# Kernel tuning notes

Hardware: AMD Instinct MI355X
Metric: run time of the kernel (lower is better)

Reference implementation:

```python
import jax, jax.numpy as jnp
import numpy as np

EPS = 1e-5

def dwconv(x, w):
    # x: (B,C,T), w: (C,1,3) depthwise, stride 1, pad 1
    return jax.lax.conv_general_dilated(
        x, w, window_strides=(1,), padding=[(1, 1)],
        dimension_numbers=('NCH', 'OIH', 'NCH'),
        feature_group_count=x.shape[1])

def chan_ln(x, w, b):
    # LayerNorm over channel dim (axis=1) of (B,C,T)
    mu = jnp.mean(x, axis=1, keepdims=True)
    r = x - mu
    sigma = jnp.mean(r * r, axis=1, keepdims=True)
    return (r / jnp.sqrt(sigma + EPS)) * w + b

def conv1x1(x, w, b):
    # x: (B,C,T), w: (O,C), b: (O,)
    return jnp.einsum('oc,bct->bot', w, x) + b[None, :, None]

def setup_inputs() -> dict:
    B, C, T, H = 4, 1024, 1024, 16
    key0 = jax.random.key(0)
    ks = jax.random.split(key0, 16)
    s = 0.02
    inp = {
        'query': jax.random.normal(ks[0], (B, C, T), jnp.float32),
        'key': jax.random.normal(ks[1], (B, C, T), jnp.float32),
        'value': jax.random.normal(ks[2], (B, C, T), jnp.float32),
        'query_mask': jnp.ones((B, 1, T), jnp.bool_),
        'kv_mask': jnp.ones((B, 1, T), jnp.bool_),
        # depthwise conv weights (C,1,3), no bias
        'qconv_w': jax.random.normal(ks[3], (C, 1, 3), jnp.float32) * s,
        'kconv_w': jax.random.normal(ks[4], (C, 1, 3), jnp.float32) * s,
        'vconv_w': jax.random.normal(ks[5], (C, 1, 3), jnp.float32) * s,
        # channel LayerNorm affine params (1,C,1)
        'qn_w': jnp.ones((1, C, 1), jnp.float32), 'qn_b': jnp.zeros((1, C, 1), jnp.float32),
        'kn_w': jnp.ones((1, C, 1), jnp.float32), 'kn_b': jnp.zeros((1, C, 1), jnp.float32),
        'vn_w': jnp.ones((1, C, 1), jnp.float32), 'vn_b': jnp.zeros((1, C, 1), jnp.float32),
        # 1x1 conv (= per-timestep linear) weights (C,C) + bias (C,)
        'wq': jax.random.normal(ks[6], (C, C), jnp.float32) * s, 'bq': jnp.zeros((C,), jnp.float32),
        'wk': jax.random.normal(ks[7], (C, C), jnp.float32) * s, 'bk': jnp.zeros((C,), jnp.float32),
        'wv': jax.random.normal(ks[8], (C, C), jnp.float32) * s, 'bv': jnp.zeros((C,), jnp.float32),
        'wp': jax.random.normal(ks[9], (C, C), jnp.float32) * s, 'bp': jnp.zeros((C,), jnp.float32),
    }
    return inp

def reference(query, key, value, query_mask, kv_mask,
              qconv_w, kconv_w, vconv_w,
              qn_w, qn_b, kn_w, kn_b, vn_w, vn_b,
              wq, bq, wk, bk, wv, bv, wp, bp):
    B, C, T = query.shape
    H = 16
    ch = C // H
    scale = 1.0 / jnp.sqrt(jnp.asarray(ch, query.dtype))
    qm = query_mask.astype(query.dtype)   # (B,1,T), stride 1 -> qx_mask == query_mask
    kvm = kv_mask.astype(query.dtype)

    q = chan_ln(dwconv(query, qconv_w) * qm, qn_w, qn_b)
    k = chan_ln(dwconv(key, kconv_w) * kvm, kn_w, kn_b)
    v = chan_ln(dwconv(value, vconv_w) * kvm, vn_w, vn_b)

    q = conv1x1(q, wq, bq)
    k = conv1x1(k, wk, bk)
    v = conv1x1(v, wv, bv)

    # (B,C,T) -> (B,H,T,ch)
    q = q.reshape(B, H, ch, T).transpose(0, 1, 3, 2)
    k = k.reshape(B, H, ch, T).transpose(0, 1, 3, 2)
    v = v.reshape(B, H, ch, T).transpose(0, 1, 3, 2)

    att = jax.nn.softmax(jnp.einsum('bhsc,bhtc->bhst', q, k) * scale, axis=-1)
    # post-softmax mask applied to V (not to scores) — faithful to the original
    vm = v * kvm[:, :, :, None]           # (B,1,T)->(B,1,T,1) broadcast over heads/ch
    out = jnp.einsum('bhst,bhtc->bhsc', att, vm)

    out = out.transpose(0, 1, 3, 2).reshape(B, C, T)
    out = conv1x1(out, wp, bp) * qm
    return out, query_mask
```

## Files before the change

kernel.cpp:

```cpp
#include <hip/hip_runtime.h>
#include <math.h>

#define B_ 4
#define C_ 1024
#define T_ 1024
#define H_ 16
#define CH_ 64
#define BCT (B_ * C_ * T_)

typedef __attribute__((ext_vector_type(8))) short s16x8;
typedef __attribute__((ext_vector_type(4))) float f32x4;
typedef unsigned short u16;

#define MFMA16(a, b, c) __builtin_amdgcn_mfma_f32_16x16x32_bf16((a), (b), (c), 0, 0, 0)

extern "C" __device__ float __ocml_native_exp2_f32(float);

__device__ __forceinline__ u16 f2bf(float f) {
    union { float f; unsigned u; } v; v.f = f;
    unsigned r = (v.u + 0x7fffu + ((v.u >> 16) & 1u)) >> 16;
    return (u16)r;
}
__device__ __forceinline__ float bf2f(u16 h) {
    union { unsigned u; float f; } v; v.u = (unsigned)h << 16; return v.f;
}

typedef __attribute__((address_space(3))) unsigned int lds_u32;
typedef __attribute__((address_space(1))) const unsigned int glb_u32;
__device__ __forceinline__ void glds16(const void* g, const void* l_wave_uniform) {
    __builtin_amdgcn_global_load_lds(
        (glb_u32*)(unsigned long long)g,
        (lds_u32*)(unsigned long long)l_wave_uniform, 16, 0, 0);
}

#define WAIT_BARRIER(N)                                   \
    asm volatile("s_waitcnt vmcnt(" #N ")" ::: "memory"); \
    __builtin_amdgcn_s_barrier();                         \
    __builtin_amdgcn_sched_barrier(0)

__global__ __launch_bounds__(512) void prep_kernel(
    const float* __restrict__ xq, const float* __restrict__ xk, const float* __restrict__ xv,
    const float* __restrict__ wq3, const float* __restrict__ wk3, const float* __restrict__ wv3,
    const int* __restrict__ qm, const int* __restrict__ kvm,
    const float* __restrict__ qnw, const float* __restrict__ qnb,
    const float* __restrict__ knw, const float* __restrict__ knb,
    const float* __restrict__ vnw, const float* __restrict__ vnb,
    u16* __restrict__ oq, u16* __restrict__ ok, u16* __restrict__ ov,
    const float* __restrict__ w0, const float* __restrict__ w1,
    const float* __restrict__ w2, const float* __restrict__ w3,
    u16* __restrict__ o0, u16* __restrict__ o1, u16* __restrict__ o2, u16* __restrict__ o3,
    float* __restrict__ tail_out, int ntail)
{
    __shared__ __align__(16) u16 tile[32 * 1032];
    __shared__ float red1[16][33], red2[16][33];
    __shared__ float musL[32], rssL[32];

    const int bid = blockIdx.x;
    if (bid >= 384) {
        if (bid >= 2432) {
            int i = (bid - 2432) * 512 + threadIdx.x;
            if (i < ntail) tail_out[i] = (qm[i] != 0) ? 1.f : 0.f;
            return;
        }
        const int b2 = bid - 384;
        const int mat = b2 >> 9;
        const float* __restrict__ w = (mat == 0) ? w0 : (mat == 1) ? w1 : (mat == 2) ? w2 : w3;
        u16* __restrict__ o = (mat == 0) ? o0 : (mat == 1) ? o1 : (mat == 2) ? o2 : o3;
        const int i = ((b2 & 511) * 512 + threadIdx.x) * 4;
        float4 v = *(const float4*)&w[i];
        uint2 p;
        p.x = (unsigned)f2bf(v.x) | ((unsigned)f2bf(v.y) << 16);
        p.y = (unsigned)f2bf(v.z) | ((unsigned)f2bf(v.w) << 16);
        *(uint2*)&o[i] = p;
        return;
    }

    const int z = bid >> 5;
    const int tensor = z >> 2, b = z & 3;
    const float* __restrict__ x   = (tensor == 0) ? xq  : (tensor == 1) ? xk  : xv;
    const float* __restrict__ w3c = (tensor == 0) ? wq3 : (tensor == 1) ? wk3 : wv3;
    const int* __restrict__ msk   = (tensor == 0) ? qm  : kvm;
    const float* __restrict__ wln = (tensor == 0) ? qnw : (tensor == 1) ? knw : vnw;
    const float* __restrict__ bln = (tensor == 0) ? qnb : (tensor == 1) ? knb : vnb;
    u16* __restrict__ xt = (tensor == 0) ? oq : (tensor == 1) ? ok : ov;

    const int t0 = (bid & 31) * 32;

    const int tl = threadIdx.x & 31, cs = threadIdx.x >> 5;
    const int t = t0 + tl;
    const float mk = (msk[b * T_ + t] != 0) ? 1.f : 0.f;

    float s1 = 0.f, s2 = 0.f;
    #pragma unroll 4
    for (int i = 0; i < 32; ++i) {
        const int c = 2 * (cs + 16 * i);
        const float* xr0 = x + ((size_t)(b * C_ + c)) * T_ + t;
        const float* xr1 = xr0 + T_;
        float xc0 = xr0[0];
        float xm0 = (t > 0)      ? xr0[-1] : 0.f;
        float xp0 = (t < T_ - 1) ? xr0[1]  : 0.f;
        float v0 = (w3c[3 * c + 0] * xm0 + w3c[3 * c + 1] * xc0 + w3c[3 * c + 2] * xp0) * mk;
        float xc1 = xr1[0];
        float xm1 = (t > 0)      ? xr1[-1] : 0.f;
        float xp1 = (t < T_ - 1) ? xr1[1]  : 0.f;
        float v1 = (w3c[3 * c + 3] * xm1 + w3c[3 * c + 4] * xc1 + w3c[3 * c + 5] * xp1) * mk;
        s1 += v0 + v1;
        s2 += v0 * v0 + v1 * v1;
        *(unsigned*)&tile[tl * 1032 + c] =
            (unsigned)f2bf(v0) | ((unsigned)f2bf(v1) << 16);
    }
    red1[cs][tl] = s1;
    red2[cs][tl] = s2;
    __syncthreads();
    if (threadIdx.x < 32) {
        float a = 0.f, q2 = 0.f;
        #pragma unroll
        for (int i = 0; i < 16; ++i) { a += red1[i][threadIdx.x]; q2 += red2[i][threadIdx.x]; }
        float m_  = a  * (1.f / C_);
        float var = q2 * (1.f / C_) - m_ * m_;
        musL[threadIdx.x] = m_;
        rssL[threadIdx.x] = rsqrtf(var + 1e-5f);
    }
    __syncthreads();

    #pragma unroll
    for (int it = 0; it < 8; ++it) {
        const int idx = it * 512 + threadIdx.x;
        const int tt = idx >> 7, c0 = (idx & 127) * 8;
        const s16x8 pv = *(const s16x8*)&tile[tt * 1032 + c0];
        const float m_ = musL[tt], rv = rssL[tt];
        const float4 w0v = *(const float4*)&wln[c0];
        const float4 w1v = *(const float4*)&wln[c0 + 4];
        const float4 b0v = *(const float4*)&bln[c0];
        const float4 b1v = *(const float4*)&bln[c0 + 4];
        uint4 o;
        float f0, f1;
        f0 = (bf2f((u16)pv[0]) - m_) * rv * w0v.x + b0v.x;
        f1 = (bf2f((u16)pv[1]) - m_) * rv * w0v.y + b0v.y;
        o.x = (unsigned)f2bf(f0) | ((unsigned)f2bf(f1) << 16);
        f0 = (bf2f((u16)pv[2]) - m_) * rv * w0v.z + b0v.z;
        f1 = (bf2f((u16)pv[3]) - m_) * rv * w0v.w + b0v.w;
        o.y = (unsigned)f2bf(f0) | ((unsigned)f2bf(f1) << 16);
        f0 = (bf2f((u16)pv[4]) - m_) * rv * w1v.x + b1v.x;
        f1 = (bf2f((u16)pv[5]) - m_) * rv * w1v.y + b1v.y;
        o.z = (unsigned)f2bf(f0) | ((unsigned)f2bf(f1) << 16);
        f0 = (bf2f((u16)pv[6]) - m_) * rv * w1v.z + b1v.z;
        f1 = (bf2f((u16)pv[7]) - m_) * rv * w1v.w + b1v.w;
        o.w = (unsigned)f2bf(f0) | ((unsigned)f2bf(f1) << 16);
        *(uint4*)&xt[((size_t)(b * T_ + t0 + tt)) * C_ + c0] = o;
    }
}

__device__ __forceinline__ void stage_slab(
    const u16* __restrict__ gA, const u16* __restrict__ gB,
    u16* lA, u16* lB, int k0, int wave, int lane)
{
    const int rw = lane >> 2, ch = lane & 3;
    const int sw = ((ch ^ ((rw >> 1) & 3)) * 8) + k0;
    const int r0 = 16 * wave + rw, r1 = r0 + 64;
    glds16(gA + (size_t)r0 * C_ + sw, lA + (16 * wave) * 32);
    glds16(gA + (size_t)r1 * C_ + sw, lA + (64 + 16 * wave) * 32);
    glds16(gB + (size_t)r0 * C_ + sw, lB + (16 * wave) * 32);
    glds16(gB + (size_t)r1 * C_ + sw, lB + (64 + 16 * wave) * 32);
}

template<int OUT_BF16>
__device__ __forceinline__ void gemm_core(
    const u16* __restrict__ A, const u16* __restrict__ B, void* __restrict__ D,
    const float* __restrict__ bias, const int* __restrict__ mask,
    float scale, int bias_on_n, int m0, int n0)
{
    __shared__ __align__(16) u16 As[3][128 * 32];
    __shared__ __align__(16) u16 Bs[3][128 * 32];
    const int tid = threadIdx.x, lane = tid & 63, wave = tid >> 6;
    const int r = lane & 15, g = lane >> 4;
    const int wm = (wave >> 1) * 64, wn = (wave & 1) * 64;
    const u16* Ab = A + (size_t)m0 * C_;
    const u16* Bb = B + (size_t)n0 * C_;

    f32x4 acc[4][4];
    #pragma unroll
    for (int i = 0; i < 4; ++i)
        #pragma unroll
        for (int j = 0; j < 4; ++j) acc[i][j] = f32x4{0.f, 0.f, 0.f, 0.f};

    stage_slab(Ab, Bb, As[0], Bs[0], 0, wave, lane);
    stage_slab(Ab, Bb, As[1], Bs[1], 32, wave, lane);
    WAIT_BARRIER(4);

    const int swz = (g ^ ((r >> 1) & 3)) * 8;
    const int NK = C_ / 32;
    int cur = 0;
    for (int kk = 0; kk < NK; ++kk) {
        int pre = cur + 2; if (pre >= 3) pre -= 3;
        if (kk + 2 < NK)
            stage_slab(Ab, Bb, As[pre], Bs[pre], (kk + 2) * 32, wave, lane);
        s16x8 af[4], bf[4];
        #pragma unroll
        for (int mi = 0; mi < 4; ++mi)
            af[mi] = *(const s16x8*)&As[cur][(wm + 16 * mi + r) * 32 + swz];
        #pragma unroll
        for (int ni = 0; ni < 4; ++ni)
            bf[ni] = *(const s16x8*)&Bs[cur][(wn + 16 * ni + r) * 32 + swz];
        #pragma unroll
        for (int mi = 0; mi < 4; ++mi)
            #pragma unroll
            for (int ni = 0; ni < 4; ++ni)
                acc[mi][ni] = MFMA16(af[mi], bf[ni], acc[mi][ni]);
        if (kk + 1 < NK) {
            if (kk + 2 < NK) { WAIT_BARRIER(4); }
            else             { WAIT_BARRIER(0); }
        }
        cur = (cur == 2) ? 0 : cur + 1;
    }

    #pragma unroll
    for (int mi = 0; mi < 4; ++mi) {
        #pragma unroll
        for (int ni = 0; ni < 4; ++ni) {
            const int n = n0 + wn + 16 * ni + r;
            float mk = 1.f;
            if (mask) mk = (mask[n] != 0) ? 1.f : 0.f;
            #pragma unroll
            for (int i = 0; i < 4; ++i) {
                const int m = m0 + wm + 16 * mi + 4 * g + i;
                float v = acc[mi][ni][i] + (bias_on_n ? bias[n] : bias[m]);
                v *= scale * mk;
                size_t o = (size_t)m * 1024 + n;
                if (OUT_BF16) ((u16*)D)[o] = f2bf(v);
                else          ((float*)D)[o] = v;
            }
        }
    }
}

__global__ __launch_bounds__(256) void gemm_qkv_kernel(
    const u16* __restrict__ Xq, const u16* __restrict__ Xk, const u16* __restrict__ Xv,
    const u16* __restrict__ Wq, const u16* __restrict__ Wk, const u16* __restrict__ Wv,
    const float* __restrict__ bq, const float* __restrict__ bk, const float* __restrict__ bv,
    u16* __restrict__ Qt, u16* __restrict__ Kt, u16* __restrict__ Vb, const int* __restrict__ kvm)
{
    const int p = blockIdx.x;
    const int lb = (p & 7) * 96 + (p >> 3);
    const int z = lb >> 6, yy = (lb >> 3) & 7, xx = lb & 7;
    const int tensor = z >> 2, b = z & 3;
    const size_t off = (size_t)b * (1024 * 1024);
    const float qscale = 0.125f * 1.44269504088896340736f;
    const u16* A = (tensor == 0) ? Xq + off : (tensor == 1) ? Xk + off : Wv;
    const u16* B = (tensor == 0) ? Wq       : (tensor == 1) ? Wk       : Xv + off;
    u16*       D = (tensor == 0) ? Qt + off : (tensor == 1) ? Kt + off : Vb + off;
    const float* bias = (tensor == 0) ? bq : (tensor == 1) ? bk : bv;
    const int* mask = (tensor == 2) ? kvm + (size_t)b * T_ : nullptr;
    gemm_core<1>(A, B, D, bias, mask, (tensor == 0) ? qscale : 1.f, tensor != 2,
                 yy * 128, xx * 128);
}

__global__ __launch_bounds__(256) void gemm_out_kernel(
    const u16* __restrict__ Wp, const u16* __restrict__ att,
    const float* __restrict__ bp, float* __restrict__ out, const int* __restrict__ qm)
{
    const int p = blockIdx.x;
    const int lb = (p & 7) * 32 + (p >> 3);
    const int b = lb >> 6, yy = (lb >> 3) & 7, xx = lb & 7;
    const size_t off = (size_t)b * (1024 * 1024);
    gemm_core<0>(Wp, att + off, out + off, bp, qm + (size_t)b * T_, 1.f, 0,
                 yy * 128, xx * 128);
}

__global__ __launch_bounds__(256) void attn_mfma_kernel(
    const u16* __restrict__ Qt, const u16* __restrict__ Kt, const u16* __restrict__ Vb,
    u16* __restrict__ att)
{
    const int p = blockIdx.x;
    const int lb = (p & 7) * 64 + (p >> 3);
    const int bh = lb >> 3, sblk = lb & 7;
    const int b = bh >> 4, h = bh & 15;
    const int lane = threadIdx.x & 63, wave = threadIdx.x >> 6;
    const int r = lane & 15, g = lane >> 4;
    const int hofs = h * 64;
    const int s0 = sblk * 128 + wave * 16;

    __shared__ __align__(16) u16 Ks[3][64 * 64];
    __shared__ __align__(16) u16 Vs[3][64 * 64];
    __shared__ __align__(16) u16 P_lds[4][2][16 * 72];

    const u16* qb0 = Qt + ((size_t)(b * T_ + s0 + r)) * C_ + hofs + g * 8;
    const s16x8 qf00 = *(const s16x8*)(qb0);
    const s16x8 qf01 = *(const s16x8*)(qb0 + 32);
    const s16x8 qf10 = *(const s16x8*)(qb0 + (size_t)64 * C_);
    const s16x8 qf11 = *(const s16x8*)(qb0 + (size_t)64 * C_ + 32);

    const int srow = lane >> 3, sch = lane & 7;
    const u16* kg = Kt + ((size_t)(b * T_)) * C_ + hofs;
    const u16* vg = Vb + ((size_t)(b * C_ + hofs)) * T_;

    auto stage = [&](int buf, int t0) {
        #pragma unroll
        for (int i = 0; i < 2; ++i) {
            const int rr = 16 * wave + 8 * i + srow;
            const int sw = (sch ^ (rr & 7)) * 8;
            glds16(kg + (size_t)(t0 + rr) * C_ + sw, &Ks[buf][(16 * wave + 8 * i) * 64]);
            glds16(vg + (size_t)rr * T_ + t0 + sw,   &Vs[buf][(16 * wave + 8 * i) * 64]);
        }
    };

    f32x4 acc0[4], acc1[4];
    #pragma unroll
    for (int ci = 0; ci < 4; ++ci) {
        acc0[ci] = f32x4{0.f, 0.f, 0.f, 0.f};
        acc1[ci] = f32x4{0.f, 0.f, 0.f, 0.f};
    }
    float l0 = 0.f, l1 = 0.f;
    u16* pw0 = &P_lds[wave][0][0];
    u16* pw1 = &P_lds[wave][1][0];

    stage(0, 0);
    stage(1, 64);
    WAIT_BARRIER(4);

    const int NT = T_ / 64;
    int cur = 0;
    for (int it = 0; it < NT; ++it) {
        int pre = cur + 2; if (pre >= 3) pre -= 3;
        if (it + 2 < NT) stage(pre, (it + 2) * 64);

        const u16* ks = Ks[cur];
        f32x4 st0[4], st1[4];
        #pragma unroll
        for (int tt = 0; tt < 4; ++tt) {
            const int row = (16 * tt + r) * 64;
            const s16x8 ka = *(const s16x8*)&ks[row + ((g ^ (r & 7)) * 8)];
            const s16x8 kb = *(const s16x8*)&ks[row + (((4 + g) ^ (r & 7)) * 8)];
            f32x4 sa = f32x4{0.f, 0.f, 0.f, 0.f};
            sa = MFMA16(ka, qf00, sa); sa = MFMA16(kb, qf01, sa); st0[tt] = sa;
            f32x4 sb = f32x4{0.f, 0.f, 0.f, 0.f};
            sb = MFMA16(ka, qf10, sb); sb = MFMA16(kb, qf11, sb); st1[tt] = sb;
        }

        #pragma unroll
        for (int tt = 0; tt < 4; ++tt) {
            float a0 = __ocml_native_exp2_f32(st0[tt][0]);
            float a1 = __ocml_native_exp2_f32(st0[tt][1]);
            float a2 = __ocml_native_exp2_f32(st0[tt][2]);
            float a3 = __ocml_native_exp2_f32(st0[tt][3]);
            l0 += (a0 + a1) + (a2 + a3);
            uint2 pk;
            pk.x = (unsigned)f2bf(a0) | ((unsigned)f2bf(a1) << 16);
            pk.y = (unsigned)f2bf(a2) | ((unsigned)f2bf(a3) << 16);
            *(uint2*)&pw0[r * 72 + 16 * tt + 4 * g] = pk;
            float b0 = __ocml_native_exp2_f32(st1[tt][0]);
            float b1 = __ocml_native_exp2_f32(st1[tt][1]);
            float b2 = __ocml_native_exp2_f32(st1[tt][2]);
            float b3 = __ocml_native_exp2_f32(st1[tt][3]);
            l1 += (b0 + b1) + (b2 + b3);
            pk.x = (unsigned)f2bf(b0) | ((unsigned)f2bf(b1) << 16);
            pk.y = (unsigned)f2bf(b2) | ((unsigned)f2bf(b3) << 16);
            *(uint2*)&pw1[r * 72 + 16 * tt + 4 * g] = pk;
        }

        const u16* vs = Vs[cur];
        #pragma unroll
        for (int kk = 0; kk < 2; ++kk) {
            const s16x8 pa0 = *(const s16x8*)&pw0[r * 72 + 32 * kk + 8 * g];
            const s16x8 pa1 = *(const s16x8*)&pw1[r * 72 + 32 * kk + 8 * g];
            #pragma unroll
            for (int ci = 0; ci < 4; ++ci) {
                const s16x8 vf = *(const s16x8*)
                    &vs[(16 * ci + r) * 64 + (((4 * kk + g) ^ (r & 7)) * 8)];
                acc0[ci] = MFMA16(pa0, vf, acc0[ci]);
                acc1[ci] = MFMA16(pa1, vf, acc1[ci]);
            }
        }

        if (it + 1 < NT) {
            if (it + 2 < NT) { WAIT_BARRIER(4); }
            else             { WAIT_BARRIER(0); }
        }
        cur = (cur == 2) ? 0 : cur + 1;
    }

    l0 += __shfl_xor(l0, 16); l0 += __shfl_xor(l0, 32);
    l1 += __shfl_xor(l1, 16); l1 += __shfl_xor(l1, 32);
    const float inv0 = 1.f / l0, inv1 = 1.f / l1;
    const float i00 = __shfl(inv0, 4 * g + 0), i01 = __shfl(inv0, 4 * g + 1);
    const float i02 = __shfl(inv0, 4 * g + 2), i03 = __shfl(inv0, 4 * g + 3);
    const float i10 = __shfl(inv1, 4 * g + 0), i11 = __shfl(inv1, 4 * g + 1);
    const float i12 = __shfl(inv1, 4 * g + 2), i13 = __shfl(inv1, 4 * g + 3);

    u16* ob = att + ((size_t)(b * T_ + s0 + 4 * g)) * C_ + hofs + r;
    #pragma unroll
    for (int ci = 0; ci < 4; ++ci) {
        ob[(size_t)0 * C_ + ci * 16] = f2bf(acc0[ci][0] * i00);
        ob[(size_t)1 * C_ + ci * 16] = f2bf(acc0[ci][1] * i01);
        ob[(size_t)2 * C_ + ci * 16] = f2bf(acc0[ci][2] * i02);
        ob[(size_t)3 * C_ + ci * 16] = f2bf(acc0[ci][3] * i03);
    }
    u16* ob1 = ob + (size_t)64 * C_;
    #pragma unroll
    for (int ci = 0; ci < 4; ++ci) {
        ob1[(size_t)0 * C_ + ci * 16] = f2bf(acc1[ci][0] * i10);
        ob1[(size_t)1 * C_ + ci * 16] = f2bf(acc1[ci][1] * i11);
        ob1[(size_t)2 * C_ + ci * 16] = f2bf(acc1[ci][2] * i12);
        ob1[(size_t)3 * C_ + ci * 16] = f2bf(acc1[ci][3] * i13);
    }
}

extern "C" void kernel_launch(void* const* d_in, const int* in_sizes, int n_in,
                              void* d_out, int out_size, void* d_ws, size_t ws_size,
                              hipStream_t stream)
{
    const float* query = (const float*)d_in[0];
    const float* key_  = (const float*)d_in[1];
    const float* value = (const float*)d_in[2];
    const int* qm  = (const int*)d_in[3];
    const int* kvm = (const int*)d_in[4];
    const float* qconv = (const float*)d_in[5];
    const float* kconv = (const float*)d_in[6];
    const float* vconv = (const float*)d_in[7];
    const float* qnw = (const float*)d_in[8];
    const float* qnb = (const float*)d_in[9];
    const float* knw = (const float*)d_in[10];
    const float* knb = (const float*)d_in[11];
    const float* vnw = (const float*)d_in[12];
    const float* vnb = (const float*)d_in[13];
    const float* wq = (const float*)d_in[14];
    const float* bq = (const float*)d_in[15];
    const float* wk = (const float*)d_in[16];
    const float* bk = (const float*)d_in[17];
    const float* wv = (const float*)d_in[18];
    const float* bv = (const float*)d_in[19];
    const float* wp = (const float*)d_in[20];
    const float* bp = (const float*)d_in[21];

    const size_t MB = 1024 * 1024;
    char* W = (char*)d_ws;
    u16* Xq  = (u16*)(W + 0 * MB);
    u16* Xk  = (u16*)(W + 8 * MB);
    u16* Xv  = (u16*)(W + 16 * MB);
    u16* Qt  = (u16*)(W + 24 * MB);
    u16* Kt  = (u16*)(W + 32 * MB);
    u16* Vb_ = (u16*)(W + 40 * MB);
    u16* att_ = (u16*)(W + 48 * MB);
    u16* wqb = (u16*)(W + 56 * MB);
    u16* wkb = (u16*)(W + 58 * MB);
    u16* wvb = (u16*)(W + 60 * MB);
    u16* wpb = (u16*)(W + 62 * MB);

    int ntail = out_size - BCT;
    if (ntail < 0) ntail = 0;

    prep_kernel<<<dim3(2440), 512, 0, stream>>>(
        query, key_, value, qconv, kconv, vconv, qm, kvm,
        qnw, qnb, knw, knb, vnw, vnb, Xq, Xk, Xv,
        wq, wk, wv, wp, wqb, wkb, wvb, wpb,
        (float*)d_out + BCT, ntail);

    gemm_qkv_kernel<<<dim3(768), 256, 0, stream>>>(
        Xq, Xk, Xv, wqb, wkb, wvb, bq, bk, bv, Qt, Kt, Vb_, kvm);

    attn_mfma_kernel<<<dim3(512), 256, 0, stream>>>(Qt, Kt, Vb_, att_);

    gemm_out_kernel<<<dim3(256), 256, 0, stream>>>(wpb, att_, bp, (float*)d_out, qm);
}
```

Measured before the change: 122.3 us.

## Replace QKV projection GEMM with 256x256-tile 512-thread kernel over flattened batch

```diff
diff --git a/kernel.cpp b/kernel.cpp
--- a/kernel.cpp
+++ b/kernel.cpp
@@ -35,6 +35,10 @@
 
 #define WAIT_BARRIER(N)                                   \
     asm volatile("s_waitcnt vmcnt(" #N ")" ::: "memory"); \
+    __builtin_amdgcn_s_barrier();                         \
+    __builtin_amdgcn_sched_barrier(0)
+
+#define BARRIER_ONLY()                                    \
     __builtin_amdgcn_s_barrier();                         \
     __builtin_amdgcn_sched_barrier(0)
 
@@ -151,6 +155,141 @@
     }
 }
 
+__global__ __launch_bounds__(512, 2) void gemm_qkv256_kernel(
+    const u16* __restrict__ Xq, const u16* __restrict__ Xk, const u16* __restrict__ Xv,
+    const u16* __restrict__ Wq, const u16* __restrict__ Wk, const u16* __restrict__ Wv,
+    const float* __restrict__ bq, const float* __restrict__ bk, const float* __restrict__ bv,
+    u16* __restrict__ Qt, u16* __restrict__ Kt, u16* __restrict__ Vb,
+    const int* __restrict__ kvm)
+{
+    const int p = blockIdx.x;
+    const int lb = (p & 7) * 24 + (p >> 3);
+    const int tensor = lb >> 6, tidx = lb & 63;
+
+    const float qscale = 0.125f * 1.44269504088896340736f;
+    const u16 *A, *Bm; u16* Dp; const float* bias; const int* mask;
+    float scale; int bias_on_n; long ldd; int m0, n0;
+    if (tensor == 0) {
+        A = Xq; Bm = Wq; Dp = Qt; bias = bq; mask = nullptr;
+        scale = qscale; bias_on_n = 1; ldd = 1024;
+        m0 = (tidx >> 2) * 256; n0 = (tidx & 3) * 256;
+    } else if (tensor == 1) {
+        A = Xk; Bm = Wk; Dp = Kt; bias = bk; mask = nullptr;
+        scale = 1.f; bias_on_n = 1; ldd = 1024;
+        m0 = (tidx >> 2) * 256; n0 = (tidx & 3) * 256;
+    } else {
+        A = Wv; Bm = Xv; Dp = Vb; bias = bv; mask = kvm;
+        scale = 1.f; bias_on_n = 0; ldd = 4096;
+        m0 = (tidx & 3) * 256; n0 = (tidx >> 2) * 256;
+    }
+
+    __shared__ __align__(16) u16 LA[2][2][128 * 64];
+    __shared__ __align__(16) u16 LB[2][2][128 * 64];
+
+    const int tid = threadIdx.x, lane = tid & 63, wave = tid >> 6;
+    const int r = lane & 15, g = lane >> 4;
+    const int wm = (wave >> 2) * 128;
+    const int wn = (wave & 3) * 64;
+    const int ha = wave >> 2;
+    const int hb = (wave & 3) >> 1;
+    const int rbB = wn & 64;
+
+    const u16* gA = A + (size_t)m0 * 1024;
+    const u16* gB = Bm + (size_t)n0 * 1024;
+    const int ccsrc = (lane & 7) ^ (((lane >> 5) & 1) << 1);
+    const int rsw = ((r >> 2) & 1) << 1;
+
+    auto stageH = [&](int H) {
+        const int kt2 = H >> 2, hsel = H & 3;
+        const int isA = hsel >> 1, hh = hsel & 1;
+        const u16* gsrc = isA ? gA : gB;
+        u16* ldst = isA ? &LA[kt2 & 1][hh][0] : &LB[kt2 & 1][hh][0];
+        #pragma unroll
+        for (int i = 0; i < 2; ++i) {
+            const int rowin = wave * 16 + i * 8;
+            const int row = hh * 128 + rowin + (lane >> 3);
+            glds16(gsrc + (size_t)row * 1024 + kt2 * 64 + ccsrc * 8,
+                   ldst + rowin * 64);
+        }
+    };
+
+    f32x4 acc[8][4];
+    #pragma unroll
+    for (int i = 0; i < 8; ++i)
+        #pragma unroll
+        for (int j = 0; j < 4; ++j) acc[i][j] = f32x4{0.f, 0.f, 0.f, 0.f};
+
+    #pragma unroll
+    for (int H = 0; H < 6; ++H) stageH(H);
+    WAIT_BARRIER(4);
+
+    for (int kt = 0; kt < 16; ++kt) {
+        const int bt = kt & 1;
+        s16x8 bfr[4][2];
+        #pragma unroll
+        for (int q = 0; q < 4; ++q) {
+            if (q == 0) {
+                #pragma unroll
+                for (int ni = 0; ni < 4; ++ni)
+                    #pragma unroll
+                    for (int ks = 0; ks < 2; ++ks) {
+                        const int row = rbB + 16 * ni + r;
+                        const int csw = (4 * ks + g) ^ rsw;
+                        bfr[ni][ks] = *(const s16x8*)&LB[bt][hb][row * 64 + csw * 8];
+                    }
+            }
+            s16x8 afr[2][2];
+            #pragma unroll
+            for (int m2 = 0; m2 < 2; ++m2)
+                #pragma unroll
+                for (int ks = 0; ks < 2; ++ks) {
+                    const int row = 16 * (2 * q + m2) + r;
+                    const int csw = (4 * ks + g) ^ rsw;
+                    afr[m2][ks] = *(const s16x8*)&LA[bt][ha][row * 64 + csw * 8];
+                }
+            const int Hs = 4 * kt + q + 6;
+            if (Hs < 64) stageH(Hs);
+            if (q == 3) {
+                if (kt < 14)       { WAIT_BARRIER(4); }
+                else if (kt == 14) { WAIT_BARRIER(0); }
+                else               { BARRIER_ONLY(); }
+            } else {
+                BARRIER_ONLY();
+            }
+            asm volatile("s_waitcnt lgkmcnt(0)" ::: "memory");
+            __builtin_amdgcn_sched_barrier(0);
+            __builtin_amdgcn_s_setprio(1);
+            #pragma unroll
+            for (int m2 = 0; m2 < 2; ++m2)
+                #pragma unroll
+                for (int ni = 0; ni < 4; ++ni) {
+                    acc[2 * q + m2][ni] = MFMA16(afr[m2][0], bfr[ni][0], acc[2 * q + m2][ni]);
+                    acc[2 * q + m2][ni] = MFMA16(afr[m2][1], bfr[ni][1], acc[2 * q + m2][ni]);
+                }
+            __builtin_amdgcn_s_setprio(0);
+            __builtin_amdgcn_sched_barrier(0);
+            BARRIER_ONLY();
+        }
+    }
+
+    #pragma unroll
+    for (int mf = 0; mf < 8; ++mf) {
+        #pragma unroll
+        for (int ni = 0; ni < 4; ++ni) {
+            const int n = n0 + wn + 16 * ni + r;
+            float mk = 1.f;
+            if (mask) mk = (mask[n] != 0) ? 1.f : 0.f;
+            #pragma unroll
+            for (int i = 0; i < 4; ++i) {
+                const int m = m0 + wm + 16 * mf + 4 * g + i;
+                float v = acc[mf][ni][i] + (bias_on_n ? bias[n] : bias[m]);
+                v *= scale * mk;
+                Dp[(size_t)m * ldd + n] = f2bf(v);
+            }
+        }
+    }
+}
+
 __device__ __forceinline__ void stage_slab(
     const u16* __restrict__ gA, const u16* __restrict__ gB,
     u16* lA, u16* lB, int k0, int wave, int lane)
@@ -164,12 +303,20 @@
     glds16(gB + (size_t)r1 * C_ + sw, lB + (64 + 16 * wave) * 32);
 }
 
-template<int OUT_BF16>
-__device__ __forceinline__ void gemm_core(
-    const u16* __restrict__ A, const u16* __restrict__ B, void* __restrict__ D,
-    const float* __restrict__ bias, const int* __restrict__ mask,
-    float scale, int bias_on_n, int m0, int n0)
+__global__ __launch_bounds__(256) void gemm_out_kernel(
+    const u16* __restrict__ Wp, const u16* __restrict__ att,
+    const float* __restrict__ bp, float* __restrict__ out, const int* __restrict__ qm)
 {
+    const int p = blockIdx.x;
+    const int lb = (p & 7) * 32 + (p >> 3);
+    const int b = lb >> 6, yy = (lb >> 3) & 7, xx = lb & 7;
+    const size_t off = (size_t)b * (1024 * 1024);
+    const int m0 = yy * 128, n0 = xx * 128;
+    const u16* A = Wp;
+    const u16* B = att + off;
+    float* D = out + off;
+    const int* mask = qm + (size_t)b * T_;
+
     __shared__ __align__(16) u16 As[3][128 * 32];
     __shared__ __align__(16) u16 Bs[3][128 * 32];
     const int tid = threadIdx.x, lane = tid & 63, wave = tid >> 6;
@@ -219,52 +366,15 @@
         #pragma unroll
         for (int ni = 0; ni < 4; ++ni) {
             const int n = n0 + wn + 16 * ni + r;
-            float mk = 1.f;
-            if (mask) mk = (mask[n] != 0) ? 1.f : 0.f;
+            const float mk = (mask[n] != 0) ? 1.f : 0.f;
             #pragma unroll
             for (int i = 0; i < 4; ++i) {
                 const int m = m0 + wm + 16 * mi + 4 * g + i;
-                float v = acc[mi][ni][i] + (bias_on_n ? bias[n] : bias[m]);
-                v *= scale * mk;
-                size_t o = (size_t)m * 1024 + n;
-                if (OUT_BF16) ((u16*)D)[o] = f2bf(v);
-                else          ((float*)D)[o] = v;
+                float v = (acc[mi][ni][i] + bp[m]) * mk;
+                D[(size_t)m * 1024 + n] = v;
             }
         }
     }
-}
-
-__global__ __launch_bounds__(256) void gemm_qkv_kernel(
-    const u16* __restrict__ Xq, const u16* __restrict__ Xk, const u16* __restrict__ Xv,
-    const u16* __restrict__ Wq, const u16* __restrict__ Wk, const u16* __restrict__ Wv,
-    const float* __restrict__ bq, const float* __restrict__ bk, const float* __restrict__ bv,
-    u16* __restrict__ Qt, u16* __restrict__ Kt, u16* __restrict__ Vb, const int* __restrict__ kvm)
-{
-    const int p = blockIdx.x;
-    const int lb = (p & 7) * 96 + (p >> 3);
-    const int z = lb >> 6, yy = (lb >> 3) & 7, xx = lb & 7;
-    const int tensor = z >> 2, b = z & 3;
-    const size_t off = (size_t)b * (1024 * 1024);
-    const float qscale = 0.125f * 1.44269504088896340736f;
-    const u16* A = (tensor == 0) ? Xq + off : (tensor == 1) ? Xk + off : Wv;
-    const u16* B = (tensor == 0) ? Wq       : (tensor == 1) ? Wk       : Xv + off;
-    u16*       D = (tensor == 0) ? Qt + off : (tensor == 1) ? Kt + off : Vb + off;
-    const float* bias = (tensor == 0) ? bq : (tensor == 1) ? bk : bv;
-    const int* mask = (tensor == 2) ? kvm + (size_t)b * T_ : nullptr;
-    gemm_core<1>(A, B, D, bias, mask, (tensor == 0) ? qscale : 1.f, tensor != 2,
-                 yy * 128, xx * 128);
-}
-
-__global__ __launch_bounds__(256) void gemm_out_kernel(
-    const u16* __restrict__ Wp, const u16* __restrict__ att,
-    const float* __restrict__ bp, float* __restrict__ out, const int* __restrict__ qm)
-{
-    const int p = blockIdx.x;
-    const int lb = (p & 7) * 32 + (p >> 3);
-    const int b = lb >> 6, yy = (lb >> 3) & 7, xx = lb & 7;
-    const size_t off = (size_t)b * (1024 * 1024);
-    gemm_core<0>(Wp, att + off, out + off, bp, qm + (size_t)b * T_, 1.f, 0,
-                 yy * 128, xx * 128);
 }
 
 __global__ __launch_bounds__(256) void attn_mfma_kernel(
@@ -292,7 +402,7 @@
 
     const int srow = lane >> 3, sch = lane & 7;
     const u16* kg = Kt + ((size_t)(b * T_)) * C_ + hofs;
-    const u16* vg = Vb + ((size_t)(b * C_ + hofs)) * T_;
+    const u16* vg = Vb + (size_t)hofs * (B_ * T_) + b * T_;
 
     auto stage = [&](int buf, int t0) {
         #pragma unroll
@@ -300,7 +410,7 @@
             const int rr = 16 * wave + 8 * i + srow;
             const int sw = (sch ^ (rr & 7)) * 8;
             glds16(kg + (size_t)(t0 + rr) * C_ + sw, &Ks[buf][(16 * wave + 8 * i) * 64]);
-            glds16(vg + (size_t)rr * T_ + t0 + sw,   &Vs[buf][(16 * wave + 8 * i) * 64]);
+            glds16(vg + (size_t)rr * (B_ * T_) + t0 + sw, &Vs[buf][(16 * wave + 8 * i) * 64]);
         }
     };
 
@@ -455,7 +565,7 @@
         wq, wk, wv, wp, wqb, wkb, wvb, wpb,
         (float*)d_out + BCT, ntail);
 
-    gemm_qkv_kernel<<<dim3(768), 256, 0, stream>>>(
+    gemm_qkv256_kernel<<<dim3(192), 512, 0, stream>>>(
         Xq, Xk, Xv, wqb, wkb, wvb, bq, bk, bv, Qt, Kt, Vb_, kvm);
 
     attn_mfma_kernel<<<dim3(512), 256, 0, stream>>>(Qt, Kt, Vb_, att_);
```

Result: slower. 125.7 us (+2.7%).
